# Performance work log

Measured on AMD Instinct MI355X. Metric: run time of the kernel, lower is better.

The kernel has to match this reference:

```python
import jax, jax.numpy as jnp
import numpy as np

NUM_HEADS = 4
HEAD_DIM = 64
BN_EPS = 1e-5

def _leaky_relu(x, slope=0.2):
    return jnp.where(x >= 0, x, slope * x)

def _gat_conv(x, W, a_src, a_dst, src, dst):
    # x: [N, F_in], W: [F_out, F_in], a_*: [H, D]; edges src/dst: [E]
    N = x.shape[0]
    h = (x @ W.T).reshape(N, NUM_HEADS, HEAD_DIM)          # [N, H, D]
    s_src = jnp.einsum('nhd,hd->nh', h, a_src)              # [N, H]
    s_dst = jnp.einsum('nhd,hd->nh', h, a_dst)              # [N, H]
    e = _leaky_relu(s_src[src] + s_dst[dst])                # [E, H]
    # segment softmax over edges grouped by dst; torch index_reduce_ starts
    # from zeros (include_self=True) -> max with 0
    e_max = jnp.maximum(jax.ops.segment_max(e, dst, num_segments=N), 0.0)
    e_exp = jnp.exp(e - e_max[dst])                         # [E, H]
    e_sum = jax.ops.segment_sum(e_exp, dst, num_segments=N) # [N, H]
    alpha = e_exp / jnp.maximum(e_sum[dst], 1e-9)           # [E, H]
    msg = h[src] * alpha[..., None]                         # [E, H, D]
    out = jax.ops.segment_sum(msg, dst, num_segments=N)     # [N, H, D]
    return out.reshape(N, NUM_HEADS * HEAD_DIM)

def _bn_eval(x, gamma, beta, mean, var):
    return (x - mean) * jax.lax.rsqrt(var + BN_EPS) * gamma + beta

def _elu(x):
    return jnp.where(x > 0, x, jnp.expm1(x))

def setup_inputs() -> dict:
    key = jax.random.key(0)
    ks = jax.random.split(key, 12)
    N, E, IN, HID, OUT = 50000, 500000, 256, 256, 64
    s = 0.05
    return {
        'x': jax.random.normal(ks[0], (N, IN), jnp.float32),
        'edge_index': jax.random.randint(ks[1], (2, E), 0, N, jnp.int64),
        'W1': jax.random.normal(ks[2], (HID, IN), jnp.float32) * s,
        'a_src1': jax.random.normal(ks[3], (NUM_HEADS, HEAD_DIM), jnp.float32) * s,
        'a_dst1': jax.random.normal(ks[4], (NUM_HEADS, HEAD_DIM), jnp.float32) * s,
        'bn1_gamma': jnp.ones((HID,), jnp.float32),
        'bn1_beta': jnp.zeros((HID,), jnp.float32),
        'bn1_mean': jnp.zeros((HID,), jnp.float32),
        'bn1_var': jnp.ones((HID,), jnp.float32),
        'W2': jax.random.normal(ks[5], (HID, HID), jnp.float32) * s,
        'a_src2': jax.random.normal(ks[6], (NUM_HEADS, HEAD_DIM), jnp.float32) * s,
        'a_dst2': jax.random.normal(ks[7], (NUM_HEADS, HEAD_DIM), jnp.float32) * s,
        'bn2_gamma': jnp.ones((HID,), jnp.float32),
        'bn2_beta': jnp.zeros((HID,), jnp.float32),
        'bn2_mean': jnp.zeros((HID,), jnp.float32),
        'bn2_var': jnp.ones((HID,), jnp.float32),
        'Wc': jax.random.normal(ks[8], (OUT, HID), jnp.float32) * s,
        'bc': jnp.zeros((OUT,), jnp.float32),
    }

def reference(x, edge_index, W1, a_src1, a_dst1, bn1_gamma, bn1_beta, bn1_mean, bn1_var,
              W2, a_src2, a_dst2, bn2_gamma, bn2_beta, bn2_mean, bn2_var, Wc, bc):
    src, dst = edge_index[0], edge_index[1]
    h = _gat_conv(x, W1, a_src1, a_dst1, src, dst)
    h = _elu(_bn_eval(h, bn1_gamma, bn1_beta, bn1_mean, bn1_var))
    h = _gat_conv(h, W2, a_src2, a_dst2, src, dst)
    h = _elu(_bn_eval(h, bn2_gamma, bn2_beta, bn2_mean, bn2_var))
    return h @ Wc.T + bc
```

## Files before the change

kernel.cpp:

```cpp
#include <hip/hip_runtime.h>

typedef __attribute__((ext_vector_type(8))) short short8;
typedef __attribute__((ext_vector_type(4))) float f32x4;

#define FF 256
#define NHEAD 4
#define HDIM 64
#define LDS_PITCH 264

__device__ __forceinline__ float bf2f(unsigned short u) {
  union { unsigned u; float f; } v; v.u = ((unsigned)u) << 16; return v.f;
}
__device__ __forceinline__ unsigned short f2bf(float f) {
  union { unsigned u; float f; } v; v.f = f;
  unsigned r = v.u + 0x7FFFu + ((v.u >> 16) & 1u);
  return (unsigned short)(r >> 16);
}

__device__ __forceinline__ short8 loadA8(const unsigned short* p) {
  return *(const short8*)p;
}
__device__ __forceinline__ short8 loadA8(const float* p) {
  f32x4 a = *(const f32x4*)p;
  f32x4 b = *(const f32x4*)(p + 4);
  short8 r;
  r[0] = (short)f2bf(a.x); r[1] = (short)f2bf(a.y);
  r[2] = (short)f2bf(a.z); r[3] = (short)f2bf(a.w);
  r[4] = (short)f2bf(b.x); r[5] = (short)f2bf(b.y);
  r[6] = (short)f2bf(b.z); r[7] = (short)f2bf(b.w);
  return r;
}

__global__ __launch_bounds__(256) void cvtw_kernel(
    const float* __restrict__ p0, int n0, const float* __restrict__ p1, int n1,
    const float* __restrict__ p2, int n2,
    unsigned short* __restrict__ o0, unsigned short* __restrict__ o1,
    unsigned short* __restrict__ o2, int* __restrict__ deg, int nz4) {
  int i = blockIdx.x * 256 + threadIdx.x;
  const float* in;
  unsigned short* out;
  int idx;
  if (i < n0) { in = p0; out = o0; idx = i; }
  else if (i < n0 + n1) { in = p1; out = o1; idx = i - n0; }
  else if (i < n0 + n1 + n2) { in = p2; out = o2; idx = i - n0 - n1; }
  else {
    int z = i - n0 - n1 - n2;
    if (z < nz4) ((int4*)deg)[z] = int4{0, 0, 0, 0};
    return;
  }
  f32x4 v = ((const f32x4*)in)[idx];
  ushort4 o;
  o.x = f2bf(v.x); o.y = f2bf(v.y); o.z = f2bf(v.z); o.w = f2bf(v.w);
  ((ushort4*)out)[idx] = o;
}

__global__ void hist_kernel(const int* __restrict__ dst, int* __restrict__ deg,
                            int E, int N) {
  int i = blockIdx.x * blockDim.x + threadIdx.x;
  if (i < E) {
    int d = dst[i];
    if ((unsigned)d < (unsigned)N) atomicAdd(&deg[d], 1);
  }
}

__global__ __launch_bounds__(256) void scan_chunks(const int* __restrict__ deg,
                                                   int* __restrict__ excl,
                                                   int* __restrict__ csum, int N) {
  __shared__ int s[256];
  int t = threadIdx.x;
  int base = blockIdx.x * 1024 + t * 4;
  int v[4];
  int sum = 0;
#pragma unroll
  for (int i = 0; i < 4; ++i) {
    v[i] = (base + i < N) ? deg[base + i] : 0;
    sum += v[i];
  }
  s[t] = sum;
  __syncthreads();
  for (int off = 1; off < 256; off <<= 1) {
    int x = (t >= off) ? s[t - off] : 0;
    __syncthreads();
    s[t] += x;
    __syncthreads();
  }
  int run = s[t] - sum;
#pragma unroll
  for (int i = 0; i < 4; ++i) {
    if (base + i < N) excl[base + i] = run;
    run += v[i];
  }
  if (t == 255) csum[blockIdx.x] = s[255];
}

__global__ __launch_bounds__(256) void finalize_rows(const int* __restrict__ excl,
                                                     const int* __restrict__ csum,
                                                     int* __restrict__ row_start,
                                                     int* __restrict__ cursor,
                                                     int N, int E) {
  int i = blockIdx.x * blockDim.x + threadIdx.x;
  int chunk = (blockIdx.x * blockDim.x) >> 10;
  int nchunks = (N + 1023) >> 10;
  int pre;
  if (nchunks <= 64) {
    int lane = threadIdx.x & 63;
    int x = (lane < chunk) ? csum[lane] : 0;
    x += __shfl_xor(x, 1);
    x += __shfl_xor(x, 2);
    x += __shfl_xor(x, 4);
    x += __shfl_xor(x, 8);
    x += __shfl_xor(x, 16);
    x += __shfl_xor(x, 32);
    pre = x;
  } else {
    pre = 0;
    for (int k = 0; k < chunk; ++k) pre += csum[k];
  }
  if (i < N) {
    int v = excl[i] + pre;
    row_start[i] = v;
    cursor[i] = v;
  }
  if (i == 0) row_start[N] = E;
}

__global__ void scatter_kernel(const int* __restrict__ src, const int* __restrict__ dst,
                               int* __restrict__ cursor, int* __restrict__ sorted_src,
                               int E, int N) {
  int i = blockIdx.x * blockDim.x + threadIdx.x;
  if (i < E) {
    int d = dst[i];
    int s = src[i];
    if ((unsigned)d < (unsigned)N) {
      int p = atomicAdd(&cursor[d], 1);
      if ((unsigned)p < (unsigned)E)
        sorted_src[p] = ((unsigned)s < (unsigned)N) ? s : 0;
    }
  }
}

template <typename AT>
__global__ __launch_bounds__(256) void gemm_main(const AT* __restrict__ A,
                                                 const unsigned short* __restrict__ B,
                                                 unsigned short* __restrict__ Cb,
                                                 const float* __restrict__ a_src,
                                                 const float* __restrict__ a_dst,
                                                 float* __restrict__ sS,
                                                 float* __restrict__ sD,
                                                 int M) {
  __shared__ unsigned short Atile[64 * LDS_PITCH];
  const int K = 256;
  int tid = threadIdx.x;
  int wave = tid >> 6;
  int lane = tid & 63;
  int row0w = blockIdx.x * 64;
  int col0 = wave * 64;
  int lr = lane & 15;
  int quad = lane >> 4;

  short8 breg[4][8];
  {
    const unsigned short* Bp0 = B + (size_t)(col0 + lr) * K + quad * 8;
#pragma unroll
    for (int t = 0; t < 4; ++t)
#pragma unroll
      for (int kk = 0; kk < 8; ++kk)
        breg[t][kk] = *(const short8*)(Bp0 + (size_t)(16 * t) * K + kk * 32);
  }

  {
#pragma unroll
    for (int pass = 0; pass < 8; ++pass) {
      int c = tid + pass * 256;
      int row = c >> 5;
      int col8 = (c & 31) * 8;
      int grow = row0w + row;
      if (grow >= M) grow = M - 1;
      short8 v = loadA8(A + (size_t)grow * K + col8);
      *(short8*)(&Atile[row * LDS_PITCH + col8]) = v;
    }
  }
  __syncthreads();

  f32x4 acc[4][4];
#pragma unroll
  for (int rt = 0; rt < 4; ++rt)
#pragma unroll
    for (int t = 0; t < 4; ++t) acc[rt][t] = f32x4{0, 0, 0, 0};

#pragma unroll
  for (int kk = 0; kk < 8; ++kk) {
    short8 a[4];
#pragma unroll
    for (int rt = 0; rt < 4; ++rt)
      a[rt] = *(const short8*)(&Atile[(rt * 16 + lr) * LDS_PITCH + quad * 8 + kk * 32]);
#pragma unroll
    for (int rt = 0; rt < 4; ++rt)
#pragma unroll
      for (int t = 0; t < 4; ++t)
        acc[rt][t] = __builtin_amdgcn_mfma_f32_16x16x32_bf16(a[rt], breg[t][kk], acc[rt][t], 0, 0, 0);
  }

#pragma unroll
  for (int rt = 0; rt < 4; ++rt) {
#pragma unroll
    for (int t = 0; t < 4; ++t) {
#pragma unroll
      for (int r = 0; r < 4; ++r) {
        int row = row0w + rt * 16 + quad * 4 + r;
        if (row < M) {
          int col = col0 + 16 * t + lr;
          Cb[(size_t)row * FF + col] = f2bf(acc[rt][t][r]);
        }
      }
    }
  }

  {
    float asv[4], adv[4];
#pragma unroll
    for (int t = 0; t < 4; ++t) {
      asv[t] = a_src[col0 + 16 * t + lr];
      adv[t] = a_dst[col0 + 16 * t + lr];
    }
#pragma unroll
    for (int rt = 0; rt < 4; ++rt) {
#pragma unroll
      for (int r = 0; r < 4; ++r) {
        float ps = acc[rt][0][r] * asv[0] + acc[rt][1][r] * asv[1] +
                   acc[rt][2][r] * asv[2] + acc[rt][3][r] * asv[3];
        float pd = acc[rt][0][r] * adv[0] + acc[rt][1][r] * adv[1] +
                   acc[rt][2][r] * adv[2] + acc[rt][3][r] * adv[3];
#pragma unroll
        for (int sft = 1; sft < 16; sft <<= 1) {
          ps += __shfl_xor(ps, sft);
          pd += __shfl_xor(pd, sft);
        }
        if (lr == 0) {
          int row = row0w + rt * 16 + quad * 4 + r;
          if (row < M) {
            sS[row * NHEAD + wave] = ps;
            sD[row * NHEAD + wave] = pd;
          }
        }
      }
    }
  }
}

__global__ __launch_bounds__(256) void gemm_head(const unsigned short* __restrict__ A,
                                                 const unsigned short* __restrict__ B,
                                                 float* __restrict__ Cf,
                                                 const float* __restrict__ bias,
                                                 int M) {
  const int K = 256;
  int wave = threadIdx.x >> 6;
  int lane = threadIdx.x & 63;
  int row0w = blockIdx.x * 256 + wave * 64;
  if (row0w >= M) return;
  int lr = lane & 15;
  int quad = lane >> 4;

  short8 breg[4][8];
  {
    const unsigned short* Bp0 = B + (size_t)lr * K + quad * 8;
#pragma unroll
    for (int t = 0; t < 4; ++t)
#pragma unroll
      for (int kk = 0; kk < 8; ++kk)
        breg[t][kk] = *(const short8*)(Bp0 + (size_t)(16 * t) * K + kk * 32);
  }

  const unsigned short* Aps[4];
#pragma unroll
  for (int rt = 0; rt < 4; ++rt) {
    int arow = row0w + rt * 16 + lr;
    if (arow >= M) arow = M - 1;
    Aps[rt] = A + (size_t)arow * K + quad * 8;
  }

  f32x4 acc[4][4];
#pragma unroll
  for (int rt = 0; rt < 4; ++rt)
#pragma unroll
    for (int t = 0; t < 4; ++t) acc[rt][t] = f32x4{0, 0, 0, 0};

#pragma unroll
  for (int kk = 0; kk < 8; ++kk) {
    short8 a[4];
#pragma unroll
    for (int rt = 0; rt < 4; ++rt) a[rt] = *(const short8*)(Aps[rt] + kk * 32);
#pragma unroll
    for (int rt = 0; rt < 4; ++rt)
#pragma unroll
      for (int t = 0; t < 4; ++t)
        acc[rt][t] = __builtin_amdgcn_mfma_f32_16x16x32_bf16(a[rt], breg[t][kk], acc[rt][t], 0, 0, 0);
  }

#pragma unroll
  for (int rt = 0; rt < 4; ++rt) {
#pragma unroll
    for (int t = 0; t < 4; ++t) {
#pragma unroll
      for (int r = 0; r < 4; ++r) {
        int row = row0w + rt * 16 + quad * 4 + r;
        if (row < M) {
          int col = 16 * t + lr;
          Cf[(size_t)row * 64 + col] = acc[rt][t][r] + bias[col];
        }
      }
    }
  }
}

__global__ __launch_bounds__(256) void aggregate_kernel(
    const unsigned short* __restrict__ hprev, const float* __restrict__ sS,
    const float* __restrict__ sD, const int* __restrict__ row_start,
    const int* __restrict__ sorted_src, const float* __restrict__ gamma,
    const float* __restrict__ beta, const float* __restrict__ mean,
    const float* __restrict__ var, unsigned short* __restrict__ hout, int N) {
  int wave = threadIdx.x >> 6;
  int lane = threadIdx.x & 63;
  int n = blockIdx.x * 4 + wave;
  if (n >= N) return;
  int hh = lane >> 4;
  int slot = lane & 15;
  int f0 = lane * 4;
  int srcBase = lane & 48;
  int jb = row_start[n];
  int je = row_start[n + 1];
  int jlast = je - 1;
  float sdv = sD[n * NHEAD + hh];
  float l = 0.f;
  float o0 = 0.f, o1 = 0.f, o2 = 0.f, o3 = 0.f;

  for (int c = jb; c < je; c += 16) {
    int j = c + slot;
    int jc = (j < jlast) ? j : jlast;
    int s = sorted_src[jc];
    float e = sS[s * NHEAD + hh] + sdv;
    e = (e >= 0.f) ? e : 0.2f * e;
    float w = (j < je) ? __expf(e) : 0.f;
    l += w;

    {
      uint2 u[8];
#pragma unroll
      for (int k = 0; k < 8; ++k) {
        int sk = __shfl(s, srcBase + k, 64);
        u[k] = *(const uint2*)(hprev + (size_t)sk * FF + f0);
      }
#pragma unroll
      for (int k = 0; k < 8; ++k) {
        float a = __shfl(w, srcBase + k, 64);
        o0 += a * __uint_as_float(u[k].x << 16);
        o1 += a * __uint_as_float(u[k].x & 0xffff0000u);
        o2 += a * __uint_as_float(u[k].y << 16);
        o3 += a * __uint_as_float(u[k].y & 0xffff0000u);
      }
    }
    if (c + 8 < je) {
      uint2 u[8];
#pragma unroll
      for (int k = 8; k < 16; ++k) {
        int sk = __shfl(s, srcBase + k, 64);
        u[k - 8] = *(const uint2*)(hprev + (size_t)sk * FF + f0);
      }
#pragma unroll
      for (int k = 8; k < 16; ++k) {
        float a = __shfl(w, srcBase + k, 64);
        o0 += a * __uint_as_float(u[k - 8].x << 16);
        o1 += a * __uint_as_float(u[k - 8].x & 0xffff0000u);
        o2 += a * __uint_as_float(u[k - 8].y << 16);
        o3 += a * __uint_as_float(u[k - 8].y & 0xffff0000u);
      }
    }
  }

  l += __shfl_xor(l, 1);
  l += __shfl_xor(l, 2);
  l += __shfl_xor(l, 4);
  l += __shfl_xor(l, 8);
  float li = 1.f / fmaxf(l, 1e-9f);

  f32x4 g = *(const f32x4*)(gamma + f0);
  f32x4 b = *(const f32x4*)(beta + f0);
  f32x4 mu = *(const f32x4*)(mean + f0);
  f32x4 vr = *(const f32x4*)(var + f0);
  float v0 = (o0 * li - mu.x) * rsqrtf(vr.x + 1e-5f) * g.x + b.x;
  float v1 = (o1 * li - mu.y) * rsqrtf(vr.y + 1e-5f) * g.y + b.y;
  float v2 = (o2 * li - mu.z) * rsqrtf(vr.z + 1e-5f) * g.z + b.z;
  float v3 = (o3 * li - mu.w) * rsqrtf(vr.w + 1e-5f) * g.w + b.w;
  v0 = (v0 > 0.f) ? v0 : expm1f(v0);
  v1 = (v1 > 0.f) ? v1 : expm1f(v1);
  v2 = (v2 > 0.f) ? v2 : expm1f(v2);
  v3 = (v3 > 0.f) ? v3 : expm1f(v3);
  ushort4 ov;
  ov.x = f2bf(v0); ov.y = f2bf(v1); ov.z = f2bf(v2); ov.w = f2bf(v3);
  *(ushort4*)(hout + (size_t)n * FF + f0) = ov;
}

extern "C" void kernel_launch(void* const* d_in, const int* in_sizes, int n_in,
                              void* d_out, int out_size, void* d_ws, size_t ws_size,
                              hipStream_t stream) {
  const float* x   = (const float*)d_in[0];
  const int* ei    = (const int*)d_in[1];
  const float* W1  = (const float*)d_in[2];
  const float* as1 = (const float*)d_in[3];
  const float* ad1 = (const float*)d_in[4];
  const float* g1  = (const float*)d_in[5];
  const float* b1  = (const float*)d_in[6];
  const float* m1  = (const float*)d_in[7];
  const float* v1  = (const float*)d_in[8];
  const float* W2  = (const float*)d_in[9];
  const float* as2 = (const float*)d_in[10];
  const float* ad2 = (const float*)d_in[11];
  const float* g2  = (const float*)d_in[12];
  const float* b2  = (const float*)d_in[13];
  const float* m2  = (const float*)d_in[14];
  const float* v2  = (const float*)d_in[15];
  const float* Wc  = (const float*)d_in[16];
  const float* bc  = (const float*)d_in[17];

  const int N = in_sizes[0] / FF;
  const int E = in_sizes[1] / 2;
  const int* srcIdx = ei;
  const int* dstIdx = ei + E;

  char* ws = (char*)d_ws;
  size_t off = 0;
  auto take = [&](size_t bytes) -> void* {
    void* p = ws + off;
    off += (bytes + 255) & ~(size_t)255;
    return p;
  };
  int* deg        = (int*)take((size_t)((N + 3) & ~3) * 4);
  int* excl       = (int*)take((size_t)N * 4);
  int* csum       = (int*)take(256 * 4);
  int* row_start  = (int*)take(((size_t)N + 1) * 4);
  int* cursor     = (int*)take((size_t)N * 4);
  int* sorted_src = (int*)take((size_t)E * 4);
  float* sS       = (float*)take((size_t)N * NHEAD * 4);
  float* sD       = (float*)take((size_t)N * NHEAD * 4);
  unsigned short* hpre = (unsigned short*)take((size_t)N * FF * 2);
  unsigned short* hact = (unsigned short*)take((size_t)N * FF * 2);
  unsigned short* w1b  = (unsigned short*)take((size_t)FF * FF * 2);
  unsigned short* w2b  = (unsigned short*)take((size_t)FF * FF * 2);
  unsigned short* wcb  = (unsigned short*)take((size_t)64 * FF * 2);

  const int tpb = 256;

  {
    int n0 = (FF * FF) / 4, n1 = (FF * FF) / 4, n2 = (64 * FF) / 4;
    int nz4 = (N + 3) / 4;
    int tot = n0 + n1 + n2 + nz4;
    cvtw_kernel<<<(tot + tpb - 1) / tpb, tpb, 0, stream>>>(W1, n0, W2, n1, Wc, n2,
                                                           w1b, w2b, wcb, deg, nz4);
  }

  hist_kernel<<<(E + tpb - 1) / tpb, tpb, 0, stream>>>(dstIdx, deg, E, N);
  int nchunks = (N + 1023) / 1024;
  scan_chunks<<<nchunks, 256, 0, stream>>>(deg, excl, csum, N);
  finalize_rows<<<(N + tpb - 1) / tpb, tpb, 0, stream>>>(excl, csum, row_start, cursor, N, E);
  scatter_kernel<<<(E + tpb - 1) / tpb, tpb, 0, stream>>>(srcIdx, dstIdx, cursor, sorted_src, E, N);

  int aggBlocks = (N + 3) / 4;
  int gemmBlocks = (N + 63) / 64;
  int headBlocks = (N + 255) / 256;

  gemm_main<float><<<gemmBlocks, 256, 0, stream>>>(x, w1b, hpre, as1, ad1, sS, sD, N);
  aggregate_kernel<<<aggBlocks, 256, 0, stream>>>(hpre, sS, sD, row_start, sorted_src,
                                                  g1, b1, m1, v1, hact, N);
  gemm_main<unsigned short><<<gemmBlocks, 256, 0, stream>>>(hact, w2b, hpre, as2, ad2,
                                                            sS, sD, N);
  aggregate_kernel<<<aggBlocks, 256, 0, stream>>>(hpre, sS, sD, row_start, sorted_src,
                                                  g2, b2, m2, v2, hact, N);
  gemm_head<<<headBlocks, 256, 0, stream>>>(hact, wcb, (float*)d_out, bc, N);
}
```

Measured before the change: 336.2 us.

## Fuse CSR build into one persistent kernel with grid-wide barriers

Replaces the four separate launches that build the CSR (histogram, chunk scan, finalize, scatter) with a single persistent kernel of 512 blocks. The phases are separated by atomic-counter grid barriers, and each thread keeps up to four edges in registers between the histogram and scatter phases so they are not reloaded. This removes launch gaps and some intermediate global traffic. It relies on all 512 blocks being resident at once, otherwise the spin barriers deadlock; the barrier counters are zeroed by the conversion kernel.

```diff
diff --git a/kernel.cpp b/kernel.cpp
--- a/kernel.cpp
+++ b/kernel.cpp
@@ -7,6 +7,7 @@
 #define NHEAD 4
 #define HDIM 64
 #define LDS_PITCH 264
+#define BUILD_GRID 512
 
 __device__ __forceinline__ float bf2f(unsigned short u) {
   union { unsigned u; float f; } v; v.u = ((unsigned)u) << 16; return v.f;
@@ -29,6 +30,23 @@
   r[4] = (short)f2bf(b.x); r[5] = (short)f2bf(b.y);
   r[6] = (short)f2bf(b.z); r[7] = (short)f2bf(b.w);
   return r;
+}
+
+__device__ __forceinline__ int aload(const int* p) {
+  return __hip_atomic_load(p, __ATOMIC_RELAXED, __HIP_MEMORY_SCOPE_AGENT);
+}
+__device__ __forceinline__ void astore(int* p, int v) {
+  __hip_atomic_store(p, v, __ATOMIC_RELAXED, __HIP_MEMORY_SCOPE_AGENT);
+}
+__device__ __forceinline__ void gbar(int* c, int target) {
+  __syncthreads();
+  if (threadIdx.x == 0) {
+    __threadfence();
+    __hip_atomic_fetch_add(c, 1, __ATOMIC_ACQ_REL, __HIP_MEMORY_SCOPE_AGENT);
+    while (__hip_atomic_load(c, __ATOMIC_ACQUIRE, __HIP_MEMORY_SCOPE_AGENT) < target)
+      __builtin_amdgcn_s_sleep(1);
+  }
+  __syncthreads();
 }
 
 __global__ __launch_bounds__(256) void cvtw_kernel(
@@ -54,87 +72,113 @@
   ((ushort4*)out)[idx] = o;
 }
 
-__global__ void hist_kernel(const int* __restrict__ dst, int* __restrict__ deg,
-                            int E, int N) {
-  int i = blockIdx.x * blockDim.x + threadIdx.x;
-  if (i < E) {
+__global__ __launch_bounds__(256) void build_kernel(
+    const int* __restrict__ src, const int* __restrict__ dst,
+    int* __restrict__ deg, int* __restrict__ csum, int* __restrict__ row_start,
+    int* __restrict__ cursor, int* __restrict__ sorted_src,
+    int* __restrict__ cnt, int E, int N) {
+  const int t = threadIdx.x;
+  const int b = blockIdx.x;
+  const int G = gridDim.x * 256;
+  const int gtid = b * 256 + t;
+  const int target = gridDim.x;
+
+  int d0 = -1, d1 = -1, d2 = -1, d3 = -1;
+  int e0 = 0, e1 = 0, e2 = 0, e3 = 0;
+  if (gtid < E)         { d0 = dst[gtid];         e0 = src[gtid]; }
+  if (gtid + G < E)     { d1 = dst[gtid + G];     e1 = src[gtid + G]; }
+  if (gtid + 2 * G < E) { d2 = dst[gtid + 2 * G]; e2 = src[gtid + 2 * G]; }
+  if (gtid + 3 * G < E) { d3 = dst[gtid + 3 * G]; e3 = src[gtid + 3 * G]; }
+
+  if ((unsigned)d0 < (unsigned)N) atomicAdd(&deg[d0], 1);
+  if ((unsigned)d1 < (unsigned)N) atomicAdd(&deg[d1], 1);
+  if ((unsigned)d2 < (unsigned)N) atomicAdd(&deg[d2], 1);
+  if ((unsigned)d3 < (unsigned)N) atomicAdd(&deg[d3], 1);
+  for (int i = gtid + 4 * G; i < E; i += G) {
     int d = dst[i];
     if ((unsigned)d < (unsigned)N) atomicAdd(&deg[d], 1);
   }
-}
-
-__global__ __launch_bounds__(256) void scan_chunks(const int* __restrict__ deg,
-                                                   int* __restrict__ excl,
-                                                   int* __restrict__ csum, int N) {
-  __shared__ int s[256];
-  int t = threadIdx.x;
-  int base = blockIdx.x * 1024 + t * 4;
-  int v[4];
-  int sum = 0;
-#pragma unroll
-  for (int i = 0; i < 4; ++i) {
-    v[i] = (base + i < N) ? deg[base + i] : 0;
-    sum += v[i];
-  }
-  s[t] = sum;
-  __syncthreads();
-  for (int off = 1; off < 256; off <<= 1) {
-    int x = (t >= off) ? s[t - off] : 0;
+  gbar(&cnt[0], target);
+
+  const int nchunks = (N + 1023) >> 10;
+  __shared__ int sm[256];
+  int v0 = 0, v1 = 0, v2 = 0, v3 = 0, run = 0;
+  if (b < nchunks) {
+    int base = b * 1024 + t * 4;
+    v0 = (base + 0 < N) ? aload(&deg[base + 0]) : 0;
+    v1 = (base + 1 < N) ? aload(&deg[base + 1]) : 0;
+    v2 = (base + 2 < N) ? aload(&deg[base + 2]) : 0;
+    v3 = (base + 3 < N) ? aload(&deg[base + 3]) : 0;
+    int sum = v0 + v1 + v2 + v3;
+    sm[t] = sum;
     __syncthreads();
-    s[t] += x;
-    __syncthreads();
-  }
-  int run = s[t] - sum;
-#pragma unroll
-  for (int i = 0; i < 4; ++i) {
-    if (base + i < N) excl[base + i] = run;
-    run += v[i];
-  }
-  if (t == 255) csum[blockIdx.x] = s[255];
-}
-
-__global__ __launch_bounds__(256) void finalize_rows(const int* __restrict__ excl,
-                                                     const int* __restrict__ csum,
-                                                     int* __restrict__ row_start,
-                                                     int* __restrict__ cursor,
-                                                     int N, int E) {
-  int i = blockIdx.x * blockDim.x + threadIdx.x;
-  int chunk = (blockIdx.x * blockDim.x) >> 10;
-  int nchunks = (N + 1023) >> 10;
-  int pre;
-  if (nchunks <= 64) {
-    int lane = threadIdx.x & 63;
-    int x = (lane < chunk) ? csum[lane] : 0;
-    x += __shfl_xor(x, 1);
-    x += __shfl_xor(x, 2);
-    x += __shfl_xor(x, 4);
-    x += __shfl_xor(x, 8);
-    x += __shfl_xor(x, 16);
-    x += __shfl_xor(x, 32);
-    pre = x;
-  } else {
-    pre = 0;
-    for (int k = 0; k < chunk; ++k) pre += csum[k];
-  }
-  if (i < N) {
-    int v = excl[i] + pre;
-    row_start[i] = v;
-    cursor[i] = v;
-  }
-  if (i == 0) row_start[N] = E;
-}
-
-__global__ void scatter_kernel(const int* __restrict__ src, const int* __restrict__ dst,
-                               int* __restrict__ cursor, int* __restrict__ sorted_src,
-                               int E, int N) {
-  int i = blockIdx.x * blockDim.x + threadIdx.x;
-  if (i < E) {
+    for (int off = 1; off < 256; off <<= 1) {
+      int x = (t >= off) ? sm[t - off] : 0;
+      __syncthreads();
+      sm[t] += x;
+      __syncthreads();
+    }
+    run = sm[t] - sum;
+    if (t == 255) astore(&csum[b], sm[255]);
+  }
+  gbar(&cnt[1], target);
+
+  if (b < nchunks) {
+    int pre;
+    if (nchunks <= 64) {
+      int lane = t & 63;
+      int x = (lane < b) ? aload(&csum[lane]) : 0;
+      x += __shfl_xor(x, 1);
+      x += __shfl_xor(x, 2);
+      x += __shfl_xor(x, 4);
+      x += __shfl_xor(x, 8);
+      x += __shfl_xor(x, 16);
+      x += __shfl_xor(x, 32);
+      pre = x;
+    } else {
+      pre = 0;
+      for (int k = 0; k < b; ++k) pre += aload(&csum[k]);
+    }
+    int base = b * 1024 + t * 4;
+    int r = run + pre;
+    if (base + 0 < N) { row_start[base + 0] = r; astore(&cursor[base + 0], r); }
+    r += v0;
+    if (base + 1 < N) { row_start[base + 1] = r; astore(&cursor[base + 1], r); }
+    r += v1;
+    if (base + 2 < N) { row_start[base + 2] = r; astore(&cursor[base + 2], r); }
+    r += v2;
+    if (base + 3 < N) { row_start[base + 3] = r; astore(&cursor[base + 3], r); }
+  }
+  if (gtid == 0) row_start[N] = E;
+  gbar(&cnt[2], target);
+
+  if ((unsigned)d0 < (unsigned)N) {
+    int p = atomicAdd(&cursor[d0], 1);
+    if ((unsigned)p < (unsigned)E)
+      sorted_src[p] = ((unsigned)e0 < (unsigned)N) ? e0 : 0;
+  }
+  if ((unsigned)d1 < (unsigned)N) {
+    int p = atomicAdd(&cursor[d1], 1);
+    if ((unsigned)p < (unsigned)E)
+      sorted_src[p] = ((unsigned)e1 < (unsigned)N) ? e1 : 0;
+  }
+  if ((unsigned)d2 < (unsigned)N) {
+    int p = atomicAdd(&cursor[d2], 1);
+    if ((unsigned)p < (unsigned)E)
+      sorted_src[p] = ((unsigned)e2 < (unsigned)N) ? e2 : 0;
+  }
+  if ((unsigned)d3 < (unsigned)N) {
+    int p = atomicAdd(&cursor[d3], 1);
+    if ((unsigned)p < (unsigned)E)
+      sorted_src[p] = ((unsigned)e3 < (unsigned)N) ? e3 : 0;
+  }
+  for (int i = gtid + 4 * G; i < E; i += G) {
     int d = dst[i];
-    int s = src[i];
+    int sv = src[i];
     if ((unsigned)d < (unsigned)N) {
       int p = atomicAdd(&cursor[d], 1);
       if ((unsigned)p < (unsigned)E)
-        sorted_src[p] = ((unsigned)s < (unsigned)N) ? s : 0;
+        sorted_src[p] = ((unsigned)sv < (unsigned)N) ? sv : 0;
     }
   }
 }
@@ -434,8 +478,9 @@
     off += (bytes + 255) & ~(size_t)255;
     return p;
   };
-  int* deg        = (int*)take((size_t)((N + 3) & ~3) * 4);
-  int* excl       = (int*)take((size_t)N * 4);
+  const int N4 = (N + 3) & ~3;
+  int* deg        = (int*)take((size_t)(N4 + 4) * 4);
+  int* cnt        = deg + N4;
   int* csum       = (int*)take(256 * 4);
   int* row_start  = (int*)take(((size_t)N + 1) * 4);
   int* cursor     = (int*)take((size_t)N * 4);
@@ -452,17 +497,14 @@
 
   {
     int n0 = (FF * FF) / 4, n1 = (FF * FF) / 4, n2 = (64 * FF) / 4;
-    int nz4 = (N + 3) / 4;
+    int nz4 = (N4 + 4) / 4;
     int tot = n0 + n1 + n2 + nz4;
     cvtw_kernel<<<(tot + tpb - 1) / tpb, tpb, 0, stream>>>(W1, n0, W2, n1, Wc, n2,
                                                            w1b, w2b, wcb, deg, nz4);
   }
 
-  hist_kernel<<<(E + tpb - 1) / tpb, tpb, 0, stream>>>(dstIdx, deg, E, N);
-  int nchunks = (N + 1023) / 1024;
-  scan_chunks<<<nchunks, 256, 0, stream>>>(deg, excl, csum, N);
-  finalize_rows<<<(N + tpb - 1) / tpb, tpb, 0, stream>>>(excl, csum, row_start, cursor, N, E);
-  scatter_kernel<<<(E + tpb - 1) / tpb, tpb, 0, stream>>>(srcIdx, dstIdx, cursor, sorted_src, E, N);
+  build_kernel<<<BUILD_GRID, 256, 0, stream>>>(srcIdx, dstIdx, deg, csum, row_start,
+                                               cursor, sorted_src, cnt, E, N);
 
   int aggBlocks = (N + 3) / 4;
   int gemmBlocks = (N + 63) / 64;
```

Measured after the change: 423.3 us. 25.9% more time.
